# Optimization experiments

Hardware: AMD Instinct MI355X
Metric: run time of the kernel (lower is better)

The kernel has to match this reference:

```python
import jax, jax.numpy as jnp
import numpy as np

N_NODES = 100000


def gcn_conv(x, src, dst, deg_inv_sqrt, W, b):
    # x: [N, Fin], src/dst: [E_total] (self-loops included), W: [Fin, Fout]
    h = x @ W                                  # [N, Fout]
    norm = deg_inv_sqrt[src] * deg_inv_sqrt[dst]  # [E_total]
    msgs = h[src] * norm[:, None]              # [E_total, Fout] gather
    out = jax.ops.segment_sum(msgs, dst, num_segments=N_NODES)  # scatter-add
    return out + b


def setup_inputs() -> dict:
    key = jax.random.key(0)
    k1, k2, k3, k4, k5, k6, k7, k8 = jax.random.split(key, 8)
    input_dim, hidden_dim, out_dim = 4, 64, 2
    n_edges = 3200000
    x = jax.random.normal(k1, (N_NODES, input_dim), dtype=jnp.float32)
    edge_index = jax.random.randint(k2, (2, n_edges), 0, N_NODES, dtype=jnp.int64)
    s1 = 1.0 / np.sqrt(input_dim)
    s2 = 1.0 / np.sqrt(hidden_dim)
    W1 = jax.random.uniform(k3, (input_dim, hidden_dim), jnp.float32, -s1, s1)
    b1 = jnp.zeros((hidden_dim,), jnp.float32)
    W2 = jax.random.uniform(k4, (hidden_dim, hidden_dim), jnp.float32, -s2, s2)
    b2 = jnp.zeros((hidden_dim,), jnp.float32)
    Wf = jax.random.uniform(k5, (hidden_dim, out_dim), jnp.float32, -s2, s2)
    bf = jax.random.uniform(k6, (out_dim,), jnp.float32, -s2, s2)
    return {"x": x, "edge_index": edge_index, "W1": W1, "b1": b1,
            "W2": W2, "b2": b2, "Wf": Wf, "bf": bf}


def reference(x, edge_index, W1, b1, W2, b2, Wf, bf):
    # Add self-loops (PyG GCNConv default)
    loop = jnp.arange(N_NODES, dtype=edge_index.dtype)
    src = jnp.concatenate([edge_index[0], loop])
    dst = jnp.concatenate([edge_index[1], loop])
    # Symmetric normalization: degree on destination after self-loops
    deg = jax.ops.segment_sum(jnp.ones_like(dst, dtype=x.dtype), dst,
                              num_segments=N_NODES)
    deg_inv_sqrt = jnp.where(deg > 0, jax.lax.rsqrt(deg), 0.0)
    h = jax.nn.relu(gcn_conv(x, src, dst, deg_inv_sqrt, W1, b1))
    h = jax.nn.relu(gcn_conv(h, src, dst, deg_inv_sqrt, W2, b2))
    return h @ Wf + bf
```

## Files before the change

kernel.cpp:

```cpp
#include <hip/hip_runtime.h>
#include <hip/hip_bf16.h>

#define N_NODES 100000
#define N_EDGES 3200000
#define NB ((N_NODES + 255) / 256)
#define NBUCKET NB
#define EPB 8192
#define NPB ((N_EDGES + EPB - 1) / EPB)
#define BCAP 11264
#define KF_BLOCKS ((N_NODES + 255) / 256)

__device__ inline unsigned f2bf(float f) {
  unsigned x = __float_as_uint(f);
  return (x + 0x7FFFu + ((x >> 16) & 1u)) >> 16;
}


__global__ void __launch_bounds__(256) k_pass1(const int* __restrict__ src,
                                               const int* __restrict__ dst,
                                               int* __restrict__ gcur,
                                               unsigned int* __restrict__ eb) {
  __shared__ int hist[NBUCKET];
  __shared__ int gbase[NBUCKET];
  int tid = threadIdx.x;
  int base = blockIdx.x * EPB;
  int cnt = min(EPB, N_EDGES - base);
  int n4 = cnt >> 2;
  for (int i = tid; i < NBUCKET; i += 256) hist[i] = 0;
  __syncthreads();
  const int4* d4 = (const int4*)(dst + base);
  const int4* s4 = (const int4*)(src + base);
  unsigned mv[32];
  unsigned short mb[32];
#pragma unroll
  for (int k = 0; k < 8; ++k) {
    int i = tid + (k << 8);
    if (i < n4) {
      int4 dv = d4[i];
      int4 sv = s4[i];
      int b0 = dv.x >> 8, b1_ = dv.y >> 8, b2 = dv.z >> 8, b3 = dv.w >> 8;
      unsigned p0 = atomicAdd(&hist[b0], 1);
      unsigned p1 = atomicAdd(&hist[b1_], 1);
      unsigned p2 = atomicAdd(&hist[b2], 1);
      unsigned p3 = atomicAdd(&hist[b3], 1);
      mv[4 * k + 0] = (unsigned)sv.x | ((unsigned)(dv.x & 255) << 17) | (p0 << 25);
      mv[4 * k + 1] = (unsigned)sv.y | ((unsigned)(dv.y & 255) << 17) | (p1 << 25);
      mv[4 * k + 2] = (unsigned)sv.z | ((unsigned)(dv.z & 255) << 17) | (p2 << 25);
      mv[4 * k + 3] = (unsigned)sv.w | ((unsigned)(dv.w & 255) << 17) | (p3 << 25);
      mb[4 * k + 0] = (unsigned short)b0;
      mb[4 * k + 1] = (unsigned short)b1_;
      mb[4 * k + 2] = (unsigned short)b2;
      mb[4 * k + 3] = (unsigned short)b3;
    } else {
      mb[4 * k + 0] = 0xFFFF; mb[4 * k + 1] = 0xFFFF;
      mb[4 * k + 2] = 0xFFFF; mb[4 * k + 3] = 0xFFFF;
    }
  }
  __syncthreads();
  for (int b = tid; b < NBUCKET; b += 256) {
    int h = hist[b];
    gbase[b] = h ? atomicAdd(&gcur[b], h) : 0;
  }
  __syncthreads();
#pragma unroll
  for (int k = 0; k < 32; ++k) {
    if (mb[k] != 0xFFFF) {
      int b = mb[k];
      unsigned v = mv[k];
      unsigned pos = (unsigned)gbase[b] + (v >> 25);
      if (pos < BCAP) eb[(size_t)b * BCAP + pos] = v & 0x01FFFFFFu;
    }
  }
}


__global__ void __launch_bounds__(256) k_part2(unsigned int* __restrict__ eb,
                                               const int* __restrict__ gcur,
                                               int* __restrict__ rs, int* __restrict__ re,
                                               float* __restrict__ dis,
                                               const float4* __restrict__ x4,
                                               float4* __restrict__ xd) {
  __shared__ int hist[256], scn[256], cur[256];
  __shared__ int wsum[4];
  __shared__ int tot;
  __shared__ unsigned int stage[BCAP];
  int b = blockIdx.x, tid = threadIdx.x;
  int lane = tid & 63, wid = tid >> 6;
  int n0 = b << 8;
  int cnt = gcur[b];
  int base = b * BCAP;
  hist[tid] = 0; cur[tid] = 0;
  __syncthreads();
  for (int i = tid; i < cnt; i += 256)
    atomicAdd(&hist[eb[base + i] >> 17], 1);
  __syncthreads();
  int n = n0 + tid;
  int deg = hist[tid];
  int slots = (n < N_NODES) ? ((deg + 1 + 7) & ~7) : 0;
  int v = slots;
#pragma unroll
  for (int off = 1; off < 64; off <<= 1) {
    int t = __shfl_up(v, off);
    if (lane >= off) v += t;
  }
  if (lane == 63) wsum[wid] = v;
  __syncthreads();
  int x = v;
#pragma unroll
  for (int w2 = 0; w2 < 3; ++w2)
    if (wid > w2) x += wsum[w2];
  int excl = x - slots;
  if (tid == 255) tot = x;
  if (n < N_NODES) {
    rs[n]  = base + excl;
    re[n]  = base + excl + deg + 1;
    float dn = rsqrtf((float)(deg + 1));
    dis[n] = dn;
    float4 xv = x4[n];
    float4 w; w.x = xv.x * dn; w.y = xv.y * dn; w.z = xv.z * dn; w.w = xv.w * dn;
    xd[n] = w;
    stage[excl] = (unsigned)n;
    for (int i = deg + 1; i < slots; ++i)
      stage[excl + i] = (unsigned)N_NODES;
  }
  if (b == 0 && tid == 0) xd[N_NODES] = make_float4(0.f, 0.f, 0.f, 0.f);
  scn[tid] = excl + 1;
  __syncthreads();
  for (int i = tid; i < cnt; i += 256) {
    unsigned v2 = eb[base + i];
    unsigned low = v2 >> 17;
    int lpos = scn[low] + atomicAdd(&cur[low], 1);
    stage[lpos] = v2 & 0x1FFFFu;
  }
  __syncthreads();
  int total = tot;
  for (int i = tid; i < total; i += 256)
    eb[base + i] = stage[i];
  if (tid < 16) {
    int gp = total + tid;
    if (gp < BCAP) eb[base + gp] = (unsigned)N_NODES;
  }
}


__global__ void __launch_bounds__(256) k_l1(const float4* __restrict__ xd,
                                            const float* __restrict__ dis,
                                            const int* __restrict__ rs,
                                            const int* __restrict__ re,
                                            const int* __restrict__ csr,
                                            const float* __restrict__ W1,
                                            const float* __restrict__ b1,
                                            unsigned int* __restrict__ h1o) {
  int gt = blockIdx.x * 256 + threadIdx.x;
  int nid = gt >> 2, p = gt & 3;
  if (nid > N_NODES) return;
  if (nid == N_NODES) {
    uint4 z = make_uint4(0u, 0u, 0u, 0u);
    uint4* op = (uint4*)(h1o + nid * 32 + p * 8);
    op[0] = z; op[1] = z;
    return;
  }
  int e0 = rs[nid];
  int it4 = ((re[nid] - e0 + 7) & ~7) >> 2;
  const int* cp = csr + e0 + p;
  float ax = 0.f, ay = 0.f, az = 0.f, aw = 0.f;
#pragma unroll 4
  for (int t = 0; t < it4; ++t) {
    int s = cp[t << 2];
    float4 v = xd[s];
    ax += v.x; ay += v.y; az += v.z; aw += v.w;
  }
  ax += __shfl_xor(ax, 1); ax += __shfl_xor(ax, 2);
  ay += __shfl_xor(ay, 1); ay += __shfl_xor(ay, 2);
  az += __shfl_xor(az, 1); az += __shfl_xor(az, 2);
  aw += __shfl_xor(aw, 1); aw += __shfl_xor(aw, 2);
  float dn = dis[nid];
  ax *= dn; ay *= dn; az *= dn; aw *= dn;
  int j0 = p << 4;
  unsigned ou[8];
#pragma unroll
  for (int j2 = 0; j2 < 8; ++j2) {
    int j = j0 + j2 * 2;
    float s0 = b1[j]     + ax * W1[j]     + ay * W1[64 + j]     + az * W1[128 + j]     + aw * W1[192 + j];
    float s1 = b1[j + 1] + ax * W1[j + 1] + ay * W1[64 + j + 1] + az * W1[128 + j + 1] + aw * W1[192 + j + 1];
    unsigned u0 = f2bf(fmaxf(s0, 0.f) * dn);
    unsigned u1 = f2bf(fmaxf(s1, 0.f) * dn);
    ou[j2] = u0 | (u1 << 16);
  }
  uint4* op = (uint4*)(h1o + nid * 32 + p * 8);
  op[0] = make_uint4(ou[0], ou[1], ou[2], ou[3]);
  op[1] = make_uint4(ou[4], ou[5], ou[6], ou[7]);
}


__device__ inline void acc_bf2(float& a0, float& a1, unsigned u) {
  a0 += __uint_as_float(u << 16);
  a1 += __uint_as_float(u & 0xffff0000u);
}

__global__ void __launch_bounds__(256)
k_agg(const __hip_bfloat16* __restrict__ h1s, const float* __restrict__ dis,
      const int* __restrict__ rs, const int* __restrict__ re,
      const int* __restrict__ csr, float* __restrict__ agg) {
  int l = threadIdx.x & 63;
  int w = threadIdx.x >> 6;
  int n = blockIdx.x * 4 + w;
  int g = l >> 3;
  int c = l & 7;

  const unsigned int* h32 = (const unsigned int*)h1s;
  int e0 = rs[n];
  int iter = (re[n] - e0 + 7) >> 3;
  const int* cb = csr + e0 + g;
  int coff = c << 2;

  float a0 = 0.f, a1 = 0.f, a2 = 0.f, a3 = 0.f;
  float a4 = 0.f, a5 = 0.f, a6 = 0.f, a7 = 0.f;
  int sc = cb[0];
  int sn = cb[8];
  uint4 u = *(const uint4*)(h32 + (sc << 5) + coff);
  for (int it = 1; it < iter; ++it) {
    int sf = cb[(it + 1) << 3];
    uint4 r = *(const uint4*)(h32 + (sn << 5) + coff);
    acc_bf2(a0, a1, u.x); acc_bf2(a2, a3, u.y);
    acc_bf2(a4, a5, u.z); acc_bf2(a6, a7, u.w);
    u = r; sn = sf;
  }
  acc_bf2(a0, a1, u.x); acc_bf2(a2, a3, u.y);
  acc_bf2(a4, a5, u.z); acc_bf2(a6, a7, u.w);

#define RED3(a) a += __shfl_xor(a, 8); a += __shfl_xor(a, 16); a += __shfl_xor(a, 32);
  RED3(a0) RED3(a1) RED3(a2) RED3(a3) RED3(a4) RED3(a5) RED3(a6) RED3(a7)
#undef RED3

  float dn = dis[n];
  if (l < 8) {
    float4 v0; v0.x = a0 * dn; v0.y = a1 * dn; v0.z = a2 * dn; v0.w = a3 * dn;
    float4 v1; v1.x = a4 * dn; v1.y = a5 * dn; v1.z = a6 * dn; v1.w = a7 * dn;
    float4* ap = (float4*)(agg + (size_t)n * 64 + (l << 3));
    ap[0] = v0; ap[1] = v1;
  }
}


__global__ void __launch_bounds__(256)
k_final(const float* __restrict__ agg, const float* __restrict__ W2,
        const float* __restrict__ b2, const float* __restrict__ Wf,
        const float* __restrict__ bf, float* __restrict__ out) {
  __shared__ float sa[256 * 64];
  int tid = threadIdx.x;
  int l = tid & 63;
  int w = tid >> 6;
  int n0 = blockIdx.x * 256;

#pragma unroll 8
  for (int i = 0; i < 64; ++i) {
    int row = (w << 6) + i;
    int n = n0 + row;
    float v = (n < N_NODES) ? agg[(size_t)n * 64 + l] : 0.f;
    sa[(row << 6) + (l ^ (row & 31))] = v;
  }
  __syncthreads();

  int nl = (w << 6) + l;
  int n = n0 + nl;
  const float* sr = sa + (nl << 6);
  int sw = nl & 31;

  float t[64];
#pragma unroll
  for (int k = 0; k < 64; ++k) t[k] = b2[k];
#pragma unroll 2
  for (int j = 0; j < 64; ++j) {
    float v = sr[j ^ sw];
#pragma unroll
    for (int k = 0; k < 64; ++k)
      t[k] = fmaf(v, W2[(j << 6) + k], t[k]);
  }

  float p0 = bf[0], p1 = bf[1];
#pragma unroll
  for (int k = 0; k < 64; ++k) {
    float tv = fmaxf(t[k], 0.f);
    p0 = fmaf(tv, Wf[k * 2 + 0], p0);
    p1 = fmaf(tv, Wf[k * 2 + 1], p1);
  }
  if (n < N_NODES) {
    out[n * 2 + 0] = p0;
    out[n * 2 + 1] = p1;
  }
}


extern "C" void kernel_launch(void* const* d_in, const int* in_sizes, int n_in,
                              void* d_out, int out_size, void* d_ws, size_t ws_size,
                              hipStream_t stream) {
  const float* x  = (const float*)d_in[0];
  const int*   ei = (const int*)d_in[1];
  const float* W1 = (const float*)d_in[2];
  const float* b1 = (const float*)d_in[3];
  const float* W2 = (const float*)d_in[4];
  const float* b2 = (const float*)d_in[5];
  const float* Wf = (const float*)d_in[6];
  const float* bf = (const float*)d_in[7];
  float* out = (float*)d_out;

  const int* srcv = ei;
  const int* dstv = ei + N_EDGES;

  char* p = (char*)d_ws;
  auto take = [&](size_t bytes) { char* r = p; p += (bytes + 255) & ~(size_t)255; return r; };
  int*          gcur = (int*)take((size_t)NBUCKET * 4);
  unsigned int* eb   = (unsigned int*)take((size_t)NBUCKET * BCAP * 4 + 512);
  int*          rs   = (int*)take((size_t)N_NODES * 4);
  int*          re   = (int*)take((size_t)N_NODES * 4);
  float*        dis  = (float*)take((size_t)N_NODES * 4);
  float4*       xd   = (float4*)take((size_t)(N_NODES + 1) * 16);
  __hip_bfloat16* h1s = (__hip_bfloat16*)take((size_t)(N_NODES + 1) * 64 * 2);
  float*        agg  = (float*)take((size_t)N_NODES * 64 * 4);

  (void)hipMemsetAsync(gcur, 0, (size_t)NBUCKET * 4, stream);
  k_pass1<<<NPB, 256, 0, stream>>>(srcv, dstv, gcur, eb);
  k_part2<<<NBUCKET, 256, 0, stream>>>(eb, gcur, rs, re, dis, (const float4*)x, xd);
  const int* csr = (const int*)eb;
  k_l1<<<((N_NODES + 1) * 4 + 255) / 256, 256, 0, stream>>>(xd, dis, rs, re, csr, W1, b1, (unsigned int*)h1s);
  k_agg<<<N_NODES / 4, 256, 0, stream>>>(h1s, dis, rs, re, csr, agg);
  k_final<<<KF_BLOCKS, 256, 0, stream>>>(agg, W2, b2, Wf, bf, out);
}
```

Measured before the change: 258.0 us.

## Store aggregation in bf16 and compute final layer with MFMA

The aggregation kernel now writes its per-node output as bf16 instead of fp32, halving that intermediate buffer's traffic. The final kernel replaces the per-thread 64x64 scalar FMA matmul, which staged rows through shared memory, with bf16 16x16x32 MFMA instructions over 16-node tiles per wave. The ReLU and the 64x2 output projection are then reduced with lane shuffles. This trades fp32 precision in the second layer's matmul input and weights for matrix-core throughput and less memory traffic.

```diff
diff --git a/kernel.cpp b/kernel.cpp
--- a/kernel.cpp
+++ b/kernel.cpp
@@ -8,7 +8,11 @@
 #define EPB 8192
 #define NPB ((N_EDGES + EPB - 1) / EPB)
 #define BCAP 11264
-#define KF_BLOCKS ((N_NODES + 255) / 256)
+#define KF_TILES (N_NODES / 16)
+#define KF_BLOCKS ((KF_TILES + 3) / 4)
+
+typedef short short8 __attribute__((ext_vector_type(8)));
+typedef float f32x4 __attribute__((ext_vector_type(4)));
 
 __device__ inline unsigned f2bf(float f) {
   unsigned x = __float_as_uint(f);
@@ -201,7 +205,7 @@
 __global__ void __launch_bounds__(256)
 k_agg(const __hip_bfloat16* __restrict__ h1s, const float* __restrict__ dis,
       const int* __restrict__ rs, const int* __restrict__ re,
-      const int* __restrict__ csr, float* __restrict__ agg) {
+      const int* __restrict__ csr, unsigned short* __restrict__ aggb) {
   int l = threadIdx.x & 63;
   int w = threadIdx.x >> 6;
   int n = blockIdx.x * 4 + w;
@@ -235,60 +239,85 @@
 
   float dn = dis[n];
   if (l < 8) {
-    float4 v0; v0.x = a0 * dn; v0.y = a1 * dn; v0.z = a2 * dn; v0.w = a3 * dn;
-    float4 v1; v1.x = a4 * dn; v1.y = a5 * dn; v1.z = a6 * dn; v1.w = a7 * dn;
-    float4* ap = (float4*)(agg + (size_t)n * 64 + (l << 3));
-    ap[0] = v0; ap[1] = v1;
+    unsigned q0 = f2bf(a0 * dn) | (f2bf(a1 * dn) << 16);
+    unsigned q1 = f2bf(a2 * dn) | (f2bf(a3 * dn) << 16);
+    unsigned q2 = f2bf(a4 * dn) | (f2bf(a5 * dn) << 16);
+    unsigned q3 = f2bf(a6 * dn) | (f2bf(a7 * dn) << 16);
+    uint4* ap = (uint4*)(aggb + (size_t)n * 64 + (l << 3));
+    *ap = make_uint4(q0, q1, q2, q3);
   }
 }
 
 
 __global__ void __launch_bounds__(256)
-k_final(const float* __restrict__ agg, const float* __restrict__ W2,
+k_final(const unsigned short* __restrict__ aggb, const float* __restrict__ W2,
         const float* __restrict__ b2, const float* __restrict__ Wf,
         const float* __restrict__ bf, float* __restrict__ out) {
-  __shared__ float sa[256 * 64];
-  int tid = threadIdx.x;
-  int l = tid & 63;
-  int w = tid >> 6;
-  int n0 = blockIdx.x * 256;
-
-#pragma unroll 8
-  for (int i = 0; i < 64; ++i) {
-    int row = (w << 6) + i;
-    int n = n0 + row;
-    float v = (n < N_NODES) ? agg[(size_t)n * 64 + l] : 0.f;
-    sa[(row << 6) + (l ^ (row & 31))] = v;
-  }
-  __syncthreads();
-
-  int nl = (w << 6) + l;
-  int n = n0 + nl;
-  const float* sr = sa + (nl << 6);
-  int sw = nl & 31;
-
-  float t[64];
-#pragma unroll
-  for (int k = 0; k < 64; ++k) t[k] = b2[k];
-#pragma unroll 2
-  for (int j = 0; j < 64; ++j) {
-    float v = sr[j ^ sw];
-#pragma unroll
-    for (int k = 0; k < 64; ++k)
-      t[k] = fmaf(v, W2[(j << 6) + k], t[k]);
-  }
-
-  float p0 = bf[0], p1 = bf[1];
-#pragma unroll
-  for (int k = 0; k < 64; ++k) {
-    float tv = fmaxf(t[k], 0.f);
-    p0 = fmaf(tv, Wf[k * 2 + 0], p0);
-    p1 = fmaf(tv, Wf[k * 2 + 1], p1);
-  }
-  if (n < N_NODES) {
-    out[n * 2 + 0] = p0;
-    out[n * 2 + 1] = p1;
-  }
+  int lane = threadIdx.x & 63;
+  int wv = (blockIdx.x << 2) + (threadIdx.x >> 6);
+  if (wv >= KF_TILES) return;
+  int n0 = wv << 4;
+  int m = lane & 15;
+  int kg = lane >> 4;
+
+  short8 bfr[2][4];
+#pragma unroll
+  for (int kt = 0; kt < 2; ++kt) {
+#pragma unroll
+    for (int nt = 0; nt < 4; ++nt) {
+      short8 t;
+#pragma unroll
+      for (int j = 0; j < 8; ++j) {
+        int k = kt * 32 + kg * 8 + j;
+        t[j] = (short)f2bf(W2[k * 64 + nt * 16 + m]);
+      }
+      bfr[kt][nt] = t;
+    }
+  }
+  const unsigned short* ar = aggb + (size_t)(n0 + m) * 64 + kg * 8;
+  short8 a0 = *(const short8*)(ar);
+  short8 a1 = *(const short8*)(ar + 32);
+
+  f32x4 z = {0.f, 0.f, 0.f, 0.f};
+  f32x4 acc0 = z, acc1 = z, acc2 = z, acc3 = z;
+  acc0 = __builtin_amdgcn_mfma_f32_16x16x32_bf16(a0, bfr[0][0], acc0, 0, 0, 0);
+  acc1 = __builtin_amdgcn_mfma_f32_16x16x32_bf16(a0, bfr[0][1], acc1, 0, 0, 0);
+  acc2 = __builtin_amdgcn_mfma_f32_16x16x32_bf16(a0, bfr[0][2], acc2, 0, 0, 0);
+  acc3 = __builtin_amdgcn_mfma_f32_16x16x32_bf16(a0, bfr[0][3], acc3, 0, 0, 0);
+  acc0 = __builtin_amdgcn_mfma_f32_16x16x32_bf16(a1, bfr[1][0], acc0, 0, 0, 0);
+  acc1 = __builtin_amdgcn_mfma_f32_16x16x32_bf16(a1, bfr[1][1], acc1, 0, 0, 0);
+  acc2 = __builtin_amdgcn_mfma_f32_16x16x32_bf16(a1, bfr[1][2], acc2, 0, 0, 0);
+  acc3 = __builtin_amdgcn_mfma_f32_16x16x32_bf16(a1, bfr[1][3], acc3, 0, 0, 0);
+
+  float p0[4] = {0.f, 0.f, 0.f, 0.f};
+  float p1[4] = {0.f, 0.f, 0.f, 0.f};
+#pragma unroll
+  for (int nt = 0; nt < 4; ++nt) {
+    int col = nt * 16 + m;
+    float bb = b2[col];
+    float w0 = Wf[col * 2 + 0];
+    float w1 = Wf[col * 2 + 1];
+    f32x4 av = (nt == 0) ? acc0 : (nt == 1) ? acc1 : (nt == 2) ? acc2 : acc3;
+#pragma unroll
+    for (int r = 0; r < 4; ++r) {
+      float tv = fmaxf(av[r] + bb, 0.f);
+      p0[r] = fmaf(tv, w0, p0[r]);
+      p1[r] = fmaf(tv, w1, p1[r]);
+    }
+  }
+#pragma unroll
+  for (int r = 0; r < 4; ++r) {
+    p0[r] += __shfl_xor(p0[r], 1); p0[r] += __shfl_xor(p0[r], 2);
+    p0[r] += __shfl_xor(p0[r], 4); p0[r] += __shfl_xor(p0[r], 8);
+    p1[r] += __shfl_xor(p1[r], 1); p1[r] += __shfl_xor(p1[r], 2);
+    p1[r] += __shfl_xor(p1[r], 4); p1[r] += __shfl_xor(p1[r], 8);
+  }
+  float bf0 = bf[0], bf1 = bf[1];
+  int rowb = n0 + kg * 4;
+  if (m == 0) *(float2*)(out + (rowb + 0) * 2) = make_float2(p0[0] + bf0, p1[0] + bf1);
+  if (m == 1) *(float2*)(out + (rowb + 1) * 2) = make_float2(p0[1] + bf0, p1[1] + bf1);
+  if (m == 2) *(float2*)(out + (rowb + 2) * 2) = make_float2(p0[2] + bf0, p1[2] + bf1);
+  if (m == 3) *(float2*)(out + (rowb + 3) * 2) = make_float2(p0[3] + bf0, p1[3] + bf1);
 }
 
 
@@ -317,13 +346,13 @@
   float*        dis  = (float*)take((size_t)N_NODES * 4);
   float4*       xd   = (float4*)take((size_t)(N_NODES + 1) * 16);
   __hip_bfloat16* h1s = (__hip_bfloat16*)take((size_t)(N_NODES + 1) * 64 * 2);
-  float*        agg  = (float*)take((size_t)N_NODES * 64 * 4);
+  unsigned short* aggb = (unsigned short*)take((size_t)N_NODES * 64 * 2);
 
   (void)hipMemsetAsync(gcur, 0, (size_t)NBUCKET * 4, stream);
   k_pass1<<<NPB, 256, 0, stream>>>(srcv, dstv, gcur, eb);
   k_part2<<<NBUCKET, 256, 0, stream>>>(eb, gcur, rs, re, dis, (const float4*)x, xd);
   const int* csr = (const int*)eb;
   k_l1<<<((N_NODES + 1) * 4 + 255) / 256, 256, 0, stream>>>(xd, dis, rs, re, csr, W1, b1, (unsigned int*)h1s);
-  k_agg<<<N_NODES / 4, 256, 0, stream>>>(h1s, dis, rs, re, csr, agg);
-  k_final<<<KF_BLOCKS, 256, 0, stream>>>(agg, W2, b2, Wf, bf, out);
-}
+  k_agg<<<N_NODES / 4, 256, 0, stream>>>(h1s, dis, rs, re, csr, aggb);
+  k_final<<<KF_BLOCKS, 256, 0, stream>>>(aggb, W2, b2, Wf, bf, out);
+}
```

Result: faster. 220.1 us (-14.7%).
